# Optimization experiments

Measured on AMD Instinct MI355X. Metric: run time of the kernel, lower is better.

The kernel has to match this reference:

```python
import jax, jax.numpy as jnp
import numpy as np

S = 2048      # total tokens
DIM = 1024    # model dim
H = 16        # attention heads
DH = 64       # head dim
BOT = 256     # bottleneck dim
NIMG = 4      # images (equal size)
L = S // NIMG # tokens per image
K = 256       # sparse_k
IH = 4        # indexer heads
ID = 16       # indexer head dim
MAXREL = 64   # hardcoded in module
NBUCK = 2 * MAXREL + 1
GH = IH * 2   # gate MLP hidden (expansion=2)


def setup_inputs() -> dict:
    key = jax.random.key(0)
    ks = jax.random.split(key, 16)
    r = lambda i, sh, s=0.02: jax.random.normal(ks[i], sh, jnp.float32) * s
    return dict(
        hidden_states=jax.random.normal(ks[0], (S, DIM), jnp.float32),
        patch_coords=jax.random.randint(ks[1], (S, 2), 0, 64, dtype=jnp.int32),
        cu_seqlens=jnp.arange(NIMG + 1, dtype=jnp.int32) * L,
        rotary_pos_emb=jax.random.uniform(ks[2], (S, DH // 2), jnp.float32) * 3.0,
        Wq_idx=r(3, (2 * IH * ID, DIM)),
        Wk_idx=r(4, (2 * IH * ID, DIM)),
        W1g=r(5, (GH, IH)), b1g=jnp.zeros((GH,), jnp.float32),
        W2g=r(6, (IH, GH)), b2g=jnp.zeros((IH,), jnp.float32),
        rpe_table=r(7, (NBUCK, IH)),
        Wqkv_d=r(8, (BOT, DIM)), bqkv_d=jnp.zeros((BOT,), jnp.float32),
        Wqkv_u=r(9, (3 * DIM, BOT)), bqkv_u=jnp.zeros((3 * DIM,), jnp.float32),
        Wp_d=r(10, (BOT, DIM)), bp_d=jnp.zeros((BOT,), jnp.float32),
        Wp_u=r(11, (DIM, BOT)), bp_u=jnp.zeros((DIM,), jnp.float32),
        scaler=jnp.ones((1,), jnp.float32),
    )


def _rotate_half(x):
    x1, x2 = jnp.split(x, 2, axis=-1)
    return jnp.concatenate([-x2, x1], axis=-1)


def reference(hidden_states, patch_coords, cu_seqlens, rotary_pos_emb,
              Wq_idx, Wk_idx, W1g, b1g, W2g, b2g, rpe_table,
              Wqkv_d, bqkv_d, Wqkv_u, bqkv_u, Wp_d, bp_d, Wp_u, bp_u, scaler):
    n = cu_seqlens.shape[0] - 1            # images (equal size L)
    Li = hidden_states.shape[0] // n
    neg = jnp.finfo(hidden_states.dtype).min

    # QKV via low-rank bottleneck
    qkv = (hidden_states @ Wqkv_d.T + bqkv_d) @ Wqkv_u.T + bqkv_u  # [S, 3*DIM]
    qkv = qkv.reshape(S, 3, H, DH)
    q, k, v = qkv[:, 0], qkv[:, 1], qkv[:, 2]                      # [S, H, DH]

    # vision RoPE (emb = cat(rpe, rpe))
    emb = jnp.concatenate([rotary_pos_emb, rotary_pos_emb], axis=-1)  # [S, DH]
    cos = jnp.cos(emb)[:, None, :]
    sin = jnpp if False else jnp.sin(emb)[:, None, :]
    q = q * cos + _rotate_half(q) * sin
    k = k * cos + _rotate_half(k) * sin

    # ---- interaction indexer, vmapped over equal-size images ----
    xs = hidden_states.reshape(n, Li, DIM)
    pos = patch_coords[:, 1].reshape(n, Li).astype(jnp.float32)
    qI = (xs @ Wq_idx.T).reshape(n, Li, 2 * IH, ID)
    kI = (xs @ Wk_idx.T).reshape(n, Li, 2 * IH, ID)
    dot = jnp.einsum('nqhd,nkhd->nqkh', qI, kI)                    # [n, L, L, 2*IH]
    data_in, gate_in = dot[..., :IH], dot[..., IH:]
    rel = jnp.clip(pos[:, :, None] - pos[:, None, :], -MAXREL, MAXREL)
    bucket = (rel + MAXREL).astype(jnp.int32)                      # [n, L, L]
    rpe = rpe_table[bucket]                                        # [n, L, L, IH]
    relu_scores = jax.nn.relu(data_in + rpe)
    g = jax.nn.sigmoid(jax.nn.relu((gate_in + rpe) @ W1g.T + b1g) @ W2g.T + b2g)
    index_scores = (relu_scores * g).sum(-1)                       # [n, L, L]

    # top-k sparse mask (0 at selected keys, -inf-ish elsewhere)
    _, topk_idx = jax.lax.top_k(index_scores, K)                   # [n, L, K]
    ni = jnp.arange(n)[:, None, None]
    ri = jnp.arange(Li)[None, :, None]
    mask_local = jnp.full((n, Li, Li), neg, hidden_states.dtype).at[ni, ri, topk_idx].set(0.0)

    # block-diagonal full mask
    mask = jnp.full((S, S), neg, hidden_states.dtype)
    for i in range(n):
        mask = mask.at[i * Li:(i + 1) * Li, i * Li:(i + 1) * Li].set(mask_local[i])

    # dense SDPA with additive mask
    att = jnp.einsum('qhd,khd->hqk', q, k) / jnp.sqrt(jnp.float32(DH)).astype(q.dtype)
    att = att + mask[None]
    p = jax.nn.softmax(att, axis=-1)
    out = jnp.einsum('hqk,khd->qhd', p, v).reshape(S, H * DH)

    final = (out @ Wp_d.T + bp_d) @ Wp_u.T + bp_u
    return final * scaler
```

## Files before the change

### kernel.cpp

```cpp
#include <hip/hip_runtime.h>
#include <hip/hip_bf16.h>

#define S_    2048
#define DIM_  1024
#define H_    16
#define DH_   64
#define BOT_  256
#define NIMG_ 4
#define LI_   512
#define K_    256
#define IH_   4
#define ID_   16
#define MAXREL_ 64
#define NBUCK_ 129
#define GH_   8
#define IDH2_ 128

typedef short bf16x8 __attribute__((ext_vector_type(8)));
typedef float f32x4  __attribute__((ext_vector_type(4)));

__device__ __forceinline__ unsigned short f2bf(float x) {
    unsigned u = __float_as_uint(x);
    return (unsigned short)((u + 0x7fffu + ((u >> 16) & 1u)) >> 16);
}
__device__ __forceinline__ float bf2f(unsigned short h) {
    return __uint_as_float(((unsigned)h) << 16);
}

#define OFF_W1_    2097152
#define OFF_WQ_    2359296
#define OFF_WK_    2490368
#define OFF_WQKVU_ 2621440
#define OFF_WPD_   3407872
#define OFF_WPU_   3670016
#define NSPLIT_    3932160

__global__ __launch_bounds__(256) void split_all_kernel(
    const float* __restrict__ hid, const float* __restrict__ wqd,
    const float* __restrict__ wq,  const float* __restrict__ wk,
    const float* __restrict__ wqu, const float* __restrict__ wpd,
    const float* __restrict__ wpu,
    unsigned short* __restrict__ hi, unsigned short* __restrict__ lo)
{
    long e = ((long)blockIdx.x * 256 + threadIdx.x) * 4;
    if (e >= NSPLIT_) return;
    const float* src; long off;
    if (e < OFF_W1_)         { src = hid; off = 0; }
    else if (e < OFF_WQ_)    { src = wqd; off = OFF_W1_; }
    else if (e < OFF_WK_)    { src = wq;  off = OFF_WQ_; }
    else if (e < OFF_WQKVU_) { src = wk;  off = OFF_WK_; }
    else if (e < OFF_WPD_)   { src = wqu; off = OFF_WQKVU_; }
    else if (e < OFF_WPU_)   { src = wpd; off = OFF_WPD_; }
    else                     { src = wpu; off = OFF_WPU_; }
    float4 v = *(const float4*)(src + (e - off));
    ushort4 h, l;
    h.x = f2bf(v.x); l.x = f2bf(v.x - bf2f(h.x));
    h.y = f2bf(v.y); l.y = f2bf(v.y - bf2f(h.y));
    h.z = f2bf(v.z); l.z = f2bf(v.z - bf2f(h.z));
    h.w = f2bf(v.w); l.w = f2bf(v.w - bf2f(h.w));
    *(ushort4*)&hi[e] = h;
    *(ushort4*)&lo[e] = l;
}

__global__ __launch_bounds__(256) void gemm_bf16x3(
    const unsigned short* __restrict__ Ah, const unsigned short* __restrict__ Al,
    const unsigned short* __restrict__ Bh, const unsigned short* __restrict__ Bl,
    const float* __restrict__ bias, const float* __restrict__ scale_ptr,
    float* __restrict__ Cf, int M, int N, int Kd)
{
    __shared__ unsigned short sAh[128 * 40], sAl[128 * 40];
    __shared__ unsigned short sBh[64 * 40],  sBl[64 * 40];
    int tid = threadIdx.x;
    int lane = tid & 63, wv = tid >> 6;
    int wr = wv >> 1, wc = wv & 1;
    int row0 = blockIdx.y * 128, col0 = blockIdx.x * 64;

    f32x4 acc[4][2];
#pragma unroll
    for (int i = 0; i < 4; i++)
#pragma unroll
        for (int j = 0; j < 2; j++) acc[i][j] = (f32x4){0.f, 0.f, 0.f, 0.f};

    int ar = tid >> 1, ac = (tid & 1) * 16;
    int br = tid >> 2, bc = (tid & 3) * 8;
    const unsigned short* gAh = Ah + (size_t)(row0 + ar) * Kd + ac;
    const unsigned short* gAl = Al + (size_t)(row0 + ar) * Kd + ac;
    const unsigned short* gBh = Bh + (size_t)(col0 + br) * Kd + bc;
    const unsigned short* gBl = Bl + (size_t)(col0 + br) * Kd + bc;
    int am = lane & 15, qk = (lane >> 4) * 8;

    for (int k0 = 0; k0 < Kd; k0 += 32) {
        __syncthreads();
        *(float4*)&sAh[ar * 40 + ac]     = *(const float4*)(gAh + k0);
        *(float4*)&sAh[ar * 40 + ac + 8] = *(const float4*)(gAh + k0 + 8);
        *(float4*)&sAl[ar * 40 + ac]     = *(const float4*)(gAl + k0);
        *(float4*)&sAl[ar * 40 + ac + 8] = *(const float4*)(gAl + k0 + 8);
        *(float4*)&sBh[br * 40 + bc]     = *(const float4*)(gBh + k0);
        *(float4*)&sBl[br * 40 + bc]     = *(const float4*)(gBl + k0);
        __syncthreads();

        bf16x8 ah[4], al[4], bh[2], bl[2];
#pragma unroll
        for (int rt = 0; rt < 4; rt++) {
            int r = wr * 64 + rt * 16 + am;
            ah[rt] = *(const bf16x8*)&sAh[r * 40 + qk];
            al[rt] = *(const bf16x8*)&sAl[r * 40 + qk];
        }
#pragma unroll
        for (int ct = 0; ct < 2; ct++) {
            int c = wc * 32 + ct * 16 + am;
            bh[ct] = *(const bf16x8*)&sBh[c * 40 + qk];
            bl[ct] = *(const bf16x8*)&sBl[c * 40 + qk];
        }
#pragma unroll
        for (int rt = 0; rt < 4; rt++)
#pragma unroll
            for (int ct = 0; ct < 2; ct++) {
                acc[rt][ct] = __builtin_amdgcn_mfma_f32_16x16x32_bf16(ah[rt], bh[ct], acc[rt][ct], 0, 0, 0);
                acc[rt][ct] = __builtin_amdgcn_mfma_f32_16x16x32_bf16(ah[rt], bl[ct], acc[rt][ct], 0, 0, 0);
                acc[rt][ct] = __builtin_amdgcn_mfma_f32_16x16x32_bf16(al[rt], bh[ct], acc[rt][ct], 0, 0, 0);
            }
    }

    float scl = scale_ptr ? *scale_ptr : 1.0f;
    int rq = (lane >> 4) * 4;
#pragma unroll
    for (int rt = 0; rt < 4; rt++)
#pragma unroll
        for (int ct = 0; ct < 2; ct++) {
            int col = col0 + wc * 32 + ct * 16 + am;
            float bz = bias ? bias[col] : 0.0f;
#pragma unroll
            for (int rg = 0; rg < 4; rg++) {
                int row = row0 + wr * 64 + rt * 16 + rq + rg;
                Cf[(size_t)row * N + col] = (acc[rt][ct][rg] + bz) * scl;
            }
        }
}

__global__ __launch_bounds__(256) void gemm64_bf16x3(
    const unsigned short* __restrict__ Ah, const unsigned short* __restrict__ Al,
    const unsigned short* __restrict__ Bh, const unsigned short* __restrict__ Bl,
    const float* __restrict__ bias_lo, const float* __restrict__ bias_hi,
    float* __restrict__ Cf, unsigned short* __restrict__ Chi,
    unsigned short* __restrict__ Clo, int M, int N, int Kd, int split_col)
{
    __shared__ unsigned short sAh[64 * 72], sAl[64 * 72];
    __shared__ unsigned short sBh[64 * 72], sBl[64 * 72];
    int tid = threadIdx.x;
    int lane = tid & 63, wv = tid >> 6;
    int wr = wv >> 1, wc = wv & 1;
    int row0 = blockIdx.y * 64, col0 = blockIdx.x * 64;

    f32x4 acc[2][2];
#pragma unroll
    for (int i = 0; i < 2; i++)
#pragma unroll
        for (int j = 0; j < 2; j++) acc[i][j] = (f32x4){0.f, 0.f, 0.f, 0.f};

    int sr = tid >> 2, sc = (tid & 3) * 16;
    const unsigned short* gAh = Ah + (size_t)(row0 + sr) * Kd + sc;
    const unsigned short* gAl = Al + (size_t)(row0 + sr) * Kd + sc;
    const unsigned short* gBh = Bh + (size_t)(col0 + sr) * Kd + sc;
    const unsigned short* gBl = Bl + (size_t)(col0 + sr) * Kd + sc;
    int am = lane & 15, qk = (lane >> 4) * 8;

    for (int k0 = 0; k0 < Kd; k0 += 64) {
        __syncthreads();
        *(float4*)&sAh[sr * 72 + sc]     = *(const float4*)(gAh + k0);
        *(float4*)&sAh[sr * 72 + sc + 8] = *(const float4*)(gAh + k0 + 8);
        *(float4*)&sAl[sr * 72 + sc]     = *(const float4*)(gAl + k0);
        *(float4*)&sAl[sr * 72 + sc + 8] = *(const float4*)(gAl + k0 + 8);
        *(float4*)&sBh[sr * 72 + sc]     = *(const float4*)(gBh + k0);
        *(float4*)&sBh[sr * 72 + sc + 8] = *(const float4*)(gBh + k0 + 8);
        *(float4*)&sBl[sr * 72 + sc]     = *(const float4*)(gBl + k0);
        *(float4*)&sBl[sr * 72 + sc + 8] = *(const float4*)(gBl + k0 + 8);
        __syncthreads();

#pragma unroll
        for (int ks = 0; ks < 2; ks++) {
            bf16x8 ah[2], al[2], bh[2], bl[2];
#pragma unroll
            for (int rt = 0; rt < 2; rt++) {
                int r = wr * 32 + rt * 16 + am;
                ah[rt] = *(const bf16x8*)&sAh[r * 72 + ks * 32 + qk];
                al[rt] = *(const bf16x8*)&sAl[r * 72 + ks * 32 + qk];
            }
#pragma unroll
            for (int ct = 0; ct < 2; ct++) {
                int c = wc * 32 + ct * 16 + am;
                bh[ct] = *(const bf16x8*)&sBh[c * 72 + ks * 32 + qk];
                bl[ct] = *(const bf16x8*)&sBl[c * 72 + ks * 32 + qk];
            }
#pragma unroll
            for (int rt = 0; rt < 2; rt++)
#pragma unroll
                for (int ct = 0; ct < 2; ct++) {
                    acc[rt][ct] = __builtin_amdgcn_mfma_f32_16x16x32_bf16(ah[rt], bh[ct], acc[rt][ct], 0, 0, 0);
                    acc[rt][ct] = __builtin_amdgcn_mfma_f32_16x16x32_bf16(ah[rt], bl[ct], acc[rt][ct], 0, 0, 0);
                    acc[rt][ct] = __builtin_amdgcn_mfma_f32_16x16x32_bf16(al[rt], bh[ct], acc[rt][ct], 0, 0, 0);
                }
        }
    }

    int rq = (lane >> 4) * 4;
#pragma unroll
    for (int rt = 0; rt < 2; rt++)
#pragma unroll
        for (int ct = 0; ct < 2; ct++) {
            int col = col0 + wc * 32 + ct * 16 + am;
#pragma unroll
            for (int rg = 0; rg < 4; rg++) {
                int row = row0 + wr * 32 + rt * 16 + rq + rg;
                float v = acc[rt][ct][rg];
                if (col < split_col) {
                    if (bias_lo) v += bias_lo[col];
                    size_t idx = (size_t)row * split_col + col;
                    unsigned short hh = f2bf(v);
                    Chi[idx] = hh;
                    Clo[idx] = f2bf(v - bf2f(hh));
                } else {
                    if (bias_hi) v += bias_hi[col - split_col];
                    Cf[(size_t)row * (N - split_col) + col - split_col] = v;
                }
            }
        }
}

__global__ __launch_bounds__(256) void ropesplit_kernel(
    const float* __restrict__ qkv, const float* __restrict__ rope,
    unsigned short* __restrict__ qkvh, unsigned short* __restrict__ qkvl)
{
    int idx = blockIdx.x * 256 + threadIdx.x;
    int d = idx & 63;
    int hh = (idx >> 6) & (H_ - 1);
    int s = idx >> 10;
    size_t base = (size_t)s * 3072 + hh * 64 + d;
    float q = qkv[base];
    float k = qkv[base + 1024];
    float v = qkv[base + 2048];
    float r = rope[s * 32 + (d & 31)];
    float c = cosf(r), sn = sinf(r);
    float qp = __shfl_xor(q, 32, 64);
    float kp = __shfl_xor(k, 32, 64);
    float sgn = (d < 32) ? -1.0f : 1.0f;
    float qr = (q * c + sgn * qp * sn) * 0.125f;
    float kr = k * c + sgn * kp * sn;
    unsigned short h1 = f2bf(qr);
    qkvh[base] = h1;            qkvl[base] = f2bf(qr - bf2f(h1));
    unsigned short h2 = f2bf(kr);
    qkvh[base + 1024] = h2;     qkvl[base + 1024] = f2bf(kr - bf2f(h2));
    unsigned short h3 = f2bf(v);
    qkvh[base + 2048] = h3;     qkvl[base + 2048] = f2bf(v - bf2f(h3));
}

__global__ __launch_bounds__(256) void score_topk_kernel(
    const float* __restrict__ qIk,
    const int* __restrict__ coords, const float* __restrict__ rpe_table,
    const float* __restrict__ W1g, const float* __restrict__ b1g,
    const float* __restrict__ W2g, const float* __restrict__ b2g,
    unsigned* __restrict__ selmask)
{
    __shared__ unsigned skeys[4][LI_];
    __shared__ int shist[4][256];
    __shared__ float srpe[NBUCK_ * IH_];
    __shared__ float sW1[GH_ * IH_], sb1[GH_], sW2[IH_ * GH_], sb2[IH_];

    int tid  = threadIdx.x;
    int lane = tid & 63;
    int wv   = tid >> 6;
    int row  = blockIdx.x * 4 + wv;
    int n    = row >> 9;

    for (int i = tid; i < NBUCK_ * IH_; i += 256) srpe[i] = rpe_table[i];
    if (tid < 32) sW1[tid] = W1g[tid];
    else if (tid < 64) sW2[tid - 32] = W2g[tid - 32];
    else if (tid < 72) sb1[tid - 64] = b1g[tid - 64];
    else if (tid < 76) sb2[tid - 72] = b2g[tid - 72];

    float4 qv[32];
    {
        const float* qrow = qIk + (size_t)row * 256;
#pragma unroll
        for (int i = 0; i < 32; i++) qv[i] = *(const float4*)(qrow + 4 * i);
    }
    int pq = coords[row * 2 + 1];
    __syncthreads();

    const float* kbase = qIk + (size_t)n * LI_ * 256 + 128;
    for (int kt = 0; kt < 8; kt++) {
        int kg = kt * 64 + lane;
        const float* krow = kbase + (size_t)kg * 256;

        float dh[8];
#pragma unroll
        for (int hh = 0; hh < 8; hh++) {
            float acc = 0.0f;
#pragma unroll
            for (int dq = 0; dq < 4; dq++) {
                float4 kv = *(const float4*)(krow + hh * 16 + dq * 4);
                float4 qq = qv[hh * 4 + dq];
                acc += qq.x * kv.x + qq.y * kv.y + qq.z * kv.z + qq.w * kv.w;
            }
            dh[hh] = acc;
        }
        int pk = coords[(n * LI_ + kg) * 2 + 1];
        int rel = pq - pk;
        rel = rel < -MAXREL_ ? -MAXREL_ : (rel > MAXREL_ ? MAXREL_ : rel);
        const float* rp = srpe + (rel + MAXREL_) * IH_;
        float t1[GH_];
#pragma unroll
        for (int g = 0; g < GH_; g++) t1[g] = sb1[g];
#pragma unroll
        for (int j = 0; j < IH_; j++) {
            float gate = dh[IH_ + j] + rp[j];
#pragma unroll
            for (int g = 0; g < GH_; g++) t1[g] += gate * sW1[g * IH_ + j];
        }
#pragma unroll
        for (int g = 0; g < GH_; g++) t1[g] = fmaxf(t1[g], 0.0f);
        float score = 0.0f;
#pragma unroll
        for (int j = 0; j < IH_; j++) {
            float t2 = sb2[j];
#pragma unroll
            for (int g = 0; g < GH_; g++) t2 += t1[g] * sW2[j * GH_ + g];
            float sg = 1.0f / (1.0f + expf(-t2));
            float rs = fmaxf(dh[j] + rp[j], 0.0f);
            score += rs * sg;
        }
        unsigned bits = __float_as_uint(score);
        skeys[wv][kg] = (bits & 0x80000000u) ? ~bits : (bits | 0x80000000u);
    }
    __syncthreads();

    unsigned pref = 0u;
    int kcur = K_;
    const unsigned himask[4] = {0u, 0xFF000000u, 0xFFFF0000u, 0xFFFFFF00u};
#pragma unroll
    for (int pass = 0; pass < 4; pass++) {
        int shift = 24 - pass * 8;
        unsigned hm = himask[pass];
        *(int4*)&shist[wv][4 * lane] = make_int4(0, 0, 0, 0);
        __syncthreads();
#pragma unroll
        for (int c = 0; c < 8; c++) {
            unsigned key = skeys[wv][c * 64 + lane];
            if ((key & hm) == pref) atomicAdd(&shist[wv][(key >> shift) & 255], 1);
        }
        __syncthreads();
        int4 b4 = *(const int4*)&shist[wv][4 * lane];
        int b[4] = {b4.x, b4.y, b4.z, b4.w};
        int t = b[0] + b[1] + b[2] + b[3];
        int Ssum = t;
#pragma unroll
        for (int off = 1; off < 64; off <<= 1) {
            int u = __shfl_down(Ssum, off, 64);
            if (lane + off < 64) Ssum += u;
        }
        int E = Ssum - t;
        int cs[5];
        cs[4] = E;
        cs[3] = b[3] + E;
        cs[2] = b[2] + cs[3];
        cs[1] = b[1] + cs[2];
        cs[0] = b[0] + cs[1];
        bool found = false;
        unsigned cpref = 0u; int ck = 0;
#pragma unroll
        for (int j = 0; j < 4; j++) {
            if (!found && cs[j] >= kcur && cs[j + 1] < kcur) {
                found = true;
                cpref = pref | ((unsigned)(4 * lane + j) << shift);
                ck = kcur - cs[j + 1];
            }
        }
        unsigned long long bm = __ballot(found);
        int src = __ffsll((long long)bm) - 1;
        pref = (unsigned)__shfl((int)cpref, src, 64);
        kcur = __shfl(ck, src, 64);
        __syncthreads();
    }
    unsigned Tu = pref;

    unsigned long long bg[8], be[8];
#pragma unroll
    for (int c = 0; c < 8; c++) {
        unsigned key = skeys[wv][c * 64 + lane];
        bg[c] = __ballot(key > Tu);
        be[c] = __ballot(key == Tu);
    }
    if (lane < 16) {
        int total_gt = 0;
#pragma unroll
        for (int c = 0; c < 8; c++) total_gt += __popcll(bg[c]);
        int base = 0;
#pragma unroll
        for (int c = 0; c < 8; c++) {
            if (2 * c < lane)     base += __popc((unsigned)be[c]);
            if (2 * c + 1 < lane) base += __popc((unsigned)(be[c] >> 32));
        }
        unsigned gw = (unsigned)(bg[lane >> 1] >> (32 * (lane & 1)));
        unsigned ew = (unsigned)(be[lane >> 1] >> (32 * (lane & 1)));
        int ne = K_ - total_gt - base;
        int pc = __popc(ew);
        int m = ne < 0 ? 0 : (ne > pc ? pc : ne);
        while (pc > m) { ew ^= (1u << (31 - __clz(ew))); pc--; }
        selmask[(size_t)row * 16 + lane] = gw | ew;
    }
}

__global__ __launch_bounds__(256) void attn_kernel(
    const unsigned short* __restrict__ qkvh, const unsigned short* __restrict__ qkvl,
    const unsigned* __restrict__ selmask,
    unsigned short* __restrict__ outh, unsigned short* __restrict__ outl)
{
    __shared__ unsigned short Qh[64 * 72],  Ql[64 * 72];
    __shared__ unsigned short Kh[64 * 72],  Kl[64 * 72];
    __shared__ unsigned short VTh[64 * 72], VTl[64 * 72];
    __shared__ unsigned short Ph[64 * 72],  Pl[64 * 72];
    __shared__ unsigned Ms[64][16];

    int b  = blockIdx.x;
    int qt = b >> 6;
    int nh = b & 63;
    int h  = nh & 15;
    int n  = nh >> 4;
    int tid = threadIdx.x;
    int lane = tid & 63, w = tid >> 6;
    int lane15 = lane & 15, quad = lane >> 4;
    int q0 = n * LI_ + qt * 64;

    for (int i = tid; i < 64 * 16; i += 256)
        Ms[i >> 4][i & 15] = selmask[(size_t)(q0 + (i >> 4)) * 16 + (i & 15)];

    {
        int r = tid >> 2, c0 = (tid & 3) * 16;
        size_t off = (size_t)(q0 + r) * 3072 + h * 64 + c0;
        *(uint4*)&Qh[r * 72 + c0]     = *(const uint4*)(qkvh + off);
        *(uint4*)&Qh[r * 72 + c0 + 8] = *(const uint4*)(qkvh + off + 8);
        *(uint4*)&Ql[r * 72 + c0]     = *(const uint4*)(qkvl + off);
        *(uint4*)&Ql[r * 72 + c0 + 8] = *(const uint4*)(qkvl + off + 8);
    }

    f32x4 o_acc[4];
#pragma unroll
    for (int i = 0; i < 4; i++) o_acc[i] = (f32x4){0.f, 0.f, 0.f, 0.f};
    float rsum[4] = {};

    for (int kt = 0; kt < 8; kt++) {
        __syncthreads();
        {
            int r = tid >> 2, c0 = (tid & 3) * 16;
            size_t off = (size_t)(n * LI_ + kt * 64 + r) * 3072 + 1024 + h * 64 + c0;
            *(uint4*)&Kh[r * 72 + c0]     = *(const uint4*)(qkvh + off);
            *(uint4*)&Kh[r * 72 + c0 + 8] = *(const uint4*)(qkvh + off + 8);
            *(uint4*)&Kl[r * 72 + c0]     = *(const uint4*)(qkvl + off);
            *(uint4*)&Kl[r * 72 + c0 + 8] = *(const uint4*)(qkvl + off + 8);
        }
        {
            int dd = lane;
            int k0 = w * 16;
            size_t off = (size_t)(n * LI_ + kt * 64 + k0) * 3072 + 2048 + h * 64 + dd;
            unsigned short hb[16], lb[16];
#pragma unroll
            for (int j = 0; j < 16; j++) {
                hb[j] = qkvh[off + (size_t)j * 3072];
                lb[j] = qkvl[off + (size_t)j * 3072];
            }
            *(uint4*)&VTh[dd * 72 + k0]     = *(uint4*)&hb[0];
            *(uint4*)&VTh[dd * 72 + k0 + 8] = *(uint4*)&hb[8];
            *(uint4*)&VTl[dd * 72 + k0]     = *(uint4*)&lb[0];
            *(uint4*)&VTl[dd * 72 + k0 + 8] = *(uint4*)&lb[8];
        }
        __syncthreads();

        f32x4 s_acc[4];
#pragma unroll
        for (int nt = 0; nt < 4; nt++) s_acc[nt] = (f32x4){0.f, 0.f, 0.f, 0.f};
        {
            bf16x8 qfh[2], qfl[2];
#pragma unroll
            for (int ks = 0; ks < 2; ks++) {
                qfh[ks] = *(const bf16x8*)&Qh[(16 * w + lane15) * 72 + ks * 32 + quad * 8];
                qfl[ks] = *(const bf16x8*)&Ql[(16 * w + lane15) * 72 + ks * 32 + quad * 8];
            }
#pragma unroll
            for (int nt = 0; nt < 4; nt++) {
#pragma unroll
                for (int ks = 0; ks < 2; ks++) {
                    bf16x8 kfh = *(const bf16x8*)&Kh[(16 * nt + lane15) * 72 + ks * 32 + quad * 8];
                    bf16x8 kfl = *(const bf16x8*)&Kl[(16 * nt + lane15) * 72 + ks * 32 + quad * 8];
                    s_acc[nt] = __builtin_amdgcn_mfma_f32_16x16x32_bf16(qfh[ks], kfh, s_acc[nt], 0, 0, 0);
                    s_acc[nt] = __builtin_amdgcn_mfma_f32_16x16x32_bf16(qfh[ks], kfl, s_acc[nt], 0, 0, 0);
                    s_acc[nt] = __builtin_amdgcn_mfma_f32_16x16x32_bf16(qfl[ks], kfh, s_acc[nt], 0, 0, 0);
                }
            }
        }

#pragma unroll
        for (int nt = 0; nt < 4; nt++) {
            int kb = kt * 64 + nt * 16 + lane15;
            int wi = kb >> 5, bit = kb & 31;
#pragma unroll
            for (int reg = 0; reg < 4; reg++) {
                int qloc = 16 * w + quad * 4 + reg;
                unsigned mw = Ms[qloc][wi];
                float p = ((mw >> bit) & 1u) ? __expf(s_acc[nt][reg]) : 0.0f;
                rsum[reg] += p;
                unsigned short ph = f2bf(p);
                Ph[qloc * 72 + nt * 16 + lane15] = ph;
                Pl[qloc * 72 + nt * 16 + lane15] = f2bf(p - bf2f(ph));
            }
        }

        {
            bf16x8 pfh[2], pfl[2];
#pragma unroll
            for (int ks = 0; ks < 2; ks++) {
                pfh[ks] = *(const bf16x8*)&Ph[(16 * w + lane15) * 72 + ks * 32 + quad * 8];
                pfl[ks] = *(const bf16x8*)&Pl[(16 * w + lane15) * 72 + ks * 32 + quad * 8];
            }
#pragma unroll
            for (int dt = 0; dt < 4; dt++) {
#pragma unroll
                for (int ks = 0; ks < 2; ks++) {
                    bf16x8 vfh = *(const bf16x8*)&VTh[(16 * dt + lane15) * 72 + ks * 32 + quad * 8];
                    bf16x8 vfl = *(const bf16x8*)&VTl[(16 * dt + lane15) * 72 + ks * 32 + quad * 8];
                    o_acc[dt] = __builtin_amdgcn_mfma_f32_16x16x32_bf16(pfh[ks], vfh, o_acc[dt], 0, 0, 0);
                    o_acc[dt] = __builtin_amdgcn_mfma_f32_16x16x32_bf16(pfh[ks], vfl, o_acc[dt], 0, 0, 0);
                    o_acc[dt] = __builtin_amdgcn_mfma_f32_16x16x32_bf16(pfl[ks], vfh, o_acc[dt], 0, 0, 0);
                }
            }
        }
    }

#pragma unroll
    for (int reg = 0; reg < 4; reg++) {
        rsum[reg] += __shfl_xor(rsum[reg], 1, 64);
        rsum[reg] += __shfl_xor(rsum[reg], 2, 64);
        rsum[reg] += __shfl_xor(rsum[reg], 4, 64);
        rsum[reg] += __shfl_xor(rsum[reg], 8, 64);
    }

#pragma unroll
    for (int dt = 0; dt < 4; dt++) {
#pragma unroll
        for (int reg = 0; reg < 4; reg++) {
            float v = o_acc[dt][reg] / rsum[reg];
            size_t ob = (size_t)(q0 + 16 * w + quad * 4 + reg) * 1024 + h * 64 + 16 * dt + lane15;
            unsigned short hh = f2bf(v);
            outh[ob] = hh;
            outl[ob] = f2bf(v - bf2f(hh));
        }
    }
}

extern "C" void kernel_launch(void* const* d_in, const int* in_sizes, int n_in,
                              void* d_out, int out_size, void* d_ws, size_t ws_size,
                              hipStream_t stream)
{
    const float* hidden  = (const float*)d_in[0];
    const int*   coords  = (const int*)d_in[1];
    const float* rope    = (const float*)d_in[3];
    const float* Wq_idx  = (const float*)d_in[4];
    const float* Wk_idx  = (const float*)d_in[5];
    const float* W1g     = (const float*)d_in[6];
    const float* b1g     = (const float*)d_in[7];
    const float* W2g     = (const float*)d_in[8];
    const float* b2g     = (const float*)d_in[9];
    const float* rpe     = (const float*)d_in[10];
    const float* Wqkv_d  = (const float*)d_in[11];
    const float* bqkv_d  = (const float*)d_in[12];
    const float* Wqkv_u  = (const float*)d_in[13];
    const float* bqkv_u  = (const float*)d_in[14];
    const float* Wp_d    = (const float*)d_in[15];
    const float* bp_d    = (const float*)d_in[16];
    const float* Wp_u    = (const float*)d_in[17];
    const float* bp_u    = (const float*)d_in[18];
    const float* scaler  = (const float*)d_in[19];
    float* out = (float*)d_out;

    unsigned short* sp_hi  = (unsigned short*)d_ws;
    unsigned short* sp_lo  = sp_hi + NSPLIT_;
    unsigned short* mid_hi = sp_lo + NSPLIT_;
    unsigned short* mid_lo = mid_hi + (size_t)S_ * BOT_;
    float* qkv = (float*)(mid_lo + (size_t)S_ * BOT_);
    float* qIk = qkv + (size_t)S_ * 3 * DIM_;
    unsigned* selmask = (unsigned*)(qIk + (size_t)S_ * 256);
    unsigned short* qkvh = (unsigned short*)(selmask + (size_t)S_ * 16);
    unsigned short* qkvl = qkvh + (size_t)S_ * 3 * DIM_;

    split_all_kernel<<<(NSPLIT_ / 4 + 255) / 256, 256, 0, stream>>>(
        hidden, Wqkv_d, Wq_idx, Wk_idx, Wqkv_u, Wp_d, Wp_u, sp_hi, sp_lo);

    gemm64_bf16x3<<<dim3(512 / 64, S_ / 64), 256, 0, stream>>>(
        sp_hi, sp_lo, sp_hi + OFF_W1_, sp_lo + OFF_W1_,
        bqkv_d, nullptr, qIk, mid_hi, mid_lo, S_, 512, DIM_, 256);

    score_topk_kernel<<<S_ / 4, 256, 0, stream>>>(
        qIk, coords, rpe, W1g, b1g, W2g, b2g, selmask);

    gemm_bf16x3<<<dim3(3 * DIM_ / 64, S_ / 128), 256, 0, stream>>>(
        mid_hi, mid_lo, sp_hi + OFF_WQKVU_, sp_lo + OFF_WQKVU_,
        bqkv_u, nullptr, qkv, S_, 3 * DIM_, BOT_);

    ropesplit_kernel<<<(S_ * H_ * 64) / 256, 256, 0, stream>>>(
        qkv, rope, qkvh, qkvl);

    attn_kernel<<<NIMG_ * H_ * 8, 256, 0, stream>>>(qkvh, qkvl, selmask, sp_hi, sp_lo);

    gemm64_bf16x3<<<dim3(BOT_ / 64, S_ / 64), 256, 0, stream>>>(
        sp_hi, sp_lo, sp_hi + OFF_WPD_, sp_lo + OFF_WPD_,
        bp_d, nullptr, nullptr, mid_hi, mid_lo, S_, BOT_, DIM_, BOT_);

    gemm_bf16x3<<<dim3(DIM_ / 64, S_ / 128), 256, 0, stream>>>(
        mid_hi, mid_lo, sp_hi + OFF_WPU_, sp_lo + OFF_WPU_,
        bp_u, scaler, out, S_, DIM_, BOT_);
}
```

Before: 290.4 us.

## Write transposed indexer keys from GEMM epilogue and drop wave-local syncs in top-k

The first bottleneck GEMM now writes the indexer-key half of its output transposed, one [n, dim, key] plane per image, into a new workspace buffer. The score kernel then reads keys so that adjacent lanes touch adjacent addresses, replacing per-lane strided float4 row reads. Query vectors move from a 32-float4 register array into shared memory, which lowers register pressure. Block-wide barriers around the per-wave histogram radix select are removed because each wave uses only its own shared slices. Risks are that the new buffer extends past the old workspace end and that correctness now relies on wave-level ordering of the shared-memory histogram accesses.

```diff
diff --git a/kernel.cpp b/kernel.cpp
--- a/kernel.cpp
+++ b/kernel.cpp
@@ -142,7 +142,8 @@
     const unsigned short* __restrict__ Ah, const unsigned short* __restrict__ Al,
     const unsigned short* __restrict__ Bh, const unsigned short* __restrict__ Bl,
     const float* __restrict__ bias_lo, const float* __restrict__ bias_hi,
-    float* __restrict__ Cf, unsigned short* __restrict__ Chi,
+    float* __restrict__ Cf, float* __restrict__ CfT,
+    unsigned short* __restrict__ Chi,
     unsigned short* __restrict__ Clo, int M, int N, int Kd, int split_col)
 {
     __shared__ unsigned short sAh[64 * 72], sAl[64 * 72];
@@ -209,17 +210,30 @@
 #pragma unroll
         for (int ct = 0; ct < 2; ct++) {
             int col = col0 + wc * 32 + ct * 16 + am;
-#pragma unroll
-            for (int rg = 0; rg < 4; rg++) {
-                int row = row0 + wr * 32 + rt * 16 + rq + rg;
-                float v = acc[rt][ct][rg];
-                if (col < split_col) {
+            if (col < split_col) {
+#pragma unroll
+                for (int rg = 0; rg < 4; rg++) {
+                    int row = row0 + wr * 32 + rt * 16 + rq + rg;
+                    float v = acc[rt][ct][rg];
                     if (bias_lo) v += bias_lo[col];
                     size_t idx = (size_t)row * split_col + col;
                     unsigned short hh = f2bf(v);
                     Chi[idx] = hh;
                     Clo[idx] = f2bf(v - bf2f(hh));
-                } else {
+                }
+            } else if (CfT && col >= split_col + 128) {
+                int d = col - split_col - 128;
+                int rowb = row0 + wr * 32 + rt * 16 + rq;
+                int n = row0 >> 9;
+                int key0 = rowb & (LI_ - 1);
+                float4 vv = make_float4(acc[rt][ct][0], acc[rt][ct][1],
+                                        acc[rt][ct][2], acc[rt][ct][3]);
+                *(float4*)&CfT[(size_t)(n * 128 + d) * LI_ + key0] = vv;
+            } else {
+#pragma unroll
+                for (int rg = 0; rg < 4; rg++) {
+                    int row = row0 + wr * 32 + rt * 16 + rq + rg;
+                    float v = acc[rt][ct][rg];
                     if (bias_hi) v += bias_hi[col - split_col];
                     Cf[(size_t)row * (N - split_col) + col - split_col] = v;
                 }
@@ -255,12 +269,13 @@
 }
 
 __global__ __launch_bounds__(256) void score_topk_kernel(
-    const float* __restrict__ qIk,
+    const float* __restrict__ qIk, const float* __restrict__ kIT,
     const int* __restrict__ coords, const float* __restrict__ rpe_table,
     const float* __restrict__ W1g, const float* __restrict__ b1g,
     const float* __restrict__ W2g, const float* __restrict__ b2g,
     unsigned* __restrict__ selmask)
 {
+    __shared__ float sqI2[4][IDH2_];
     __shared__ unsigned skeys[4][LI_];
     __shared__ int shist[4][256];
     __shared__ float srpe[NBUCK_ * IH_];
@@ -277,20 +292,18 @@
     else if (tid < 64) sW2[tid - 32] = W2g[tid - 32];
     else if (tid < 72) sb1[tid - 64] = b1g[tid - 64];
     else if (tid < 76) sb2[tid - 72] = b2g[tid - 72];
-
-    float4 qv[32];
-    {
-        const float* qrow = qIk + (size_t)row * 256;
-#pragma unroll
-        for (int i = 0; i < 32; i++) qv[i] = *(const float4*)(qrow + 4 * i);
-    }
+    for (int i = tid; i < 4 * IDH2_; i += 256)
+        sqI2[i >> 7][i & 127] =
+            qIk[(size_t)(blockIdx.x * 4 + (i >> 7)) * 256 + (i & 127)];
     int pq = coords[row * 2 + 1];
     __syncthreads();
 
-    const float* kbase = qIk + (size_t)n * LI_ * 256 + 128;
+    const float* kb = kIT + (size_t)n * 128 * LI_;
+    const float* sq = &sqI2[wv][0];
+
     for (int kt = 0; kt < 8; kt++) {
         int kg = kt * 64 + lane;
-        const float* krow = kbase + (size_t)kg * 256;
+        const float* kp = kb + kg;
 
         float dh[8];
 #pragma unroll
@@ -298,9 +311,13 @@
             float acc = 0.0f;
 #pragma unroll
             for (int dq = 0; dq < 4; dq++) {
-                float4 kv = *(const float4*)(krow + hh * 16 + dq * 4);
-                float4 qq = qv[hh * 4 + dq];
-                acc += qq.x * kv.x + qq.y * kv.y + qq.z * kv.z + qq.w * kv.w;
+                int d = hh * 16 + dq * 4;
+                float k0 = kp[(size_t)(d + 0) * LI_];
+                float k1 = kp[(size_t)(d + 1) * LI_];
+                float k2 = kp[(size_t)(d + 2) * LI_];
+                float k3 = kp[(size_t)(d + 3) * LI_];
+                acc += sq[d + 0] * k0 + sq[d + 1] * k1 +
+                       sq[d + 2] * k2 + sq[d + 3] * k3;
             }
             dh[hh] = acc;
         }
@@ -332,7 +349,6 @@
         unsigned bits = __float_as_uint(score);
         skeys[wv][kg] = (bits & 0x80000000u) ? ~bits : (bits | 0x80000000u);
     }
-    __syncthreads();
 
     unsigned pref = 0u;
     int kcur = K_;
@@ -342,13 +358,11 @@
         int shift = 24 - pass * 8;
         unsigned hm = himask[pass];
         *(int4*)&shist[wv][4 * lane] = make_int4(0, 0, 0, 0);
-        __syncthreads();
 #pragma unroll
         for (int c = 0; c < 8; c++) {
             unsigned key = skeys[wv][c * 64 + lane];
             if ((key & hm) == pref) atomicAdd(&shist[wv][(key >> shift) & 255], 1);
         }
-        __syncthreads();
         int4 b4 = *(const int4*)&shist[wv][4 * lane];
         int b[4] = {b4.x, b4.y, b4.z, b4.w};
         int t = b[0] + b[1] + b[2] + b[3];
@@ -379,7 +393,6 @@
         int src = __ffsll((long long)bm) - 1;
         pref = (unsigned)__shfl((int)cpref, src, 64);
         kcur = __shfl(ck, src, 64);
-        __syncthreads();
     }
     unsigned Tu = pref;
 
@@ -590,16 +603,17 @@
     unsigned* selmask = (unsigned*)(qIk + (size_t)S_ * 256);
     unsigned short* qkvh = (unsigned short*)(selmask + (size_t)S_ * 16);
     unsigned short* qkvl = qkvh + (size_t)S_ * 3 * DIM_;
+    float* kIT = (float*)(qkvl + (size_t)S_ * 3 * DIM_);
 
     split_all_kernel<<<(NSPLIT_ / 4 + 255) / 256, 256, 0, stream>>>(
         hidden, Wqkv_d, Wq_idx, Wk_idx, Wqkv_u, Wp_d, Wp_u, sp_hi, sp_lo);
 
     gemm64_bf16x3<<<dim3(512 / 64, S_ / 64), 256, 0, stream>>>(
         sp_hi, sp_lo, sp_hi + OFF_W1_, sp_lo + OFF_W1_,
-        bqkv_d, nullptr, qIk, mid_hi, mid_lo, S_, 512, DIM_, 256);
+        bqkv_d, nullptr, qIk, kIT, mid_hi, mid_lo, S_, 512, DIM_, 256);
 
     score_topk_kernel<<<S_ / 4, 256, 0, stream>>>(
-        qIk, coords, rpe, W1g, b1g, W2g, b2g, selmask);
+        qIk, kIT, coords, rpe, W1g, b1g, W2g, b2g, selmask);
 
     gemm_bf16x3<<<dim3(3 * DIM_ / 64, S_ / 128), 256, 0, stream>>>(
         mid_hi, mid_lo, sp_hi + OFF_WQKVU_, sp_lo + OFF_WQKVU_,
@@ -612,7 +626,7 @@
 
     gemm64_bf16x3<<<dim3(BOT_ / 64, S_ / 64), 256, 0, stream>>>(
         sp_hi, sp_lo, sp_hi + OFF_WPD_, sp_lo + OFF_WPD_,
-        bp_d, nullptr, nullptr, mid_hi, mid_lo, S_, BOT_, DIM_, BOT_);
+        bp_d, nullptr, nullptr, nullptr, mid_hi, mid_lo, S_, BOT_, DIM_, BOT_);
 
     gemm_bf16x3<<<dim3(DIM_ / 64, S_ / 128), 256, 0, stream>>>(
         mid_hi, mid_lo, sp_hi + OFF_WPU_, sp_lo + OFF_WPU_,
```

After: 356.2 us. 22.7% more time.

## Stage indexer key tiles in shared memory with double buffering in score_topk

Applied to the files above, without the earlier changes.

The score_topk kernel now loads 32-key tiles of indexer keys into double-buffered shared memory, shared by all four waves of a block, instead of each wave streaming its keys from global memory. Each half-wave computes four of the eight head dot products, and the halves swap results with cross-lane shuffles. The query row is staged in LDS rather than kept in 128 registers, which frees registers. The per-wave radix-select histogram passes drop their block-wide barriers, and the kernel launch moves after the rope kernel. The trade-off is two barriers per tile and a gate MLP that both half-waves compute redundantly.

```diff
diff --git a/kernel.cpp b/kernel.cpp
--- a/kernel.cpp
+++ b/kernel.cpp
@@ -261,6 +261,8 @@
     const float* __restrict__ W2g, const float* __restrict__ b2g,
     unsigned* __restrict__ selmask)
 {
+    __shared__ float skI[2][32 * 132];
+    __shared__ float sqI2[4][IDH2_];
     __shared__ unsigned skeys[4][LI_];
     __shared__ int shist[4][256];
     __shared__ float srpe[NBUCK_ * IH_];
@@ -277,33 +279,64 @@
     else if (tid < 64) sW2[tid - 32] = W2g[tid - 32];
     else if (tid < 72) sb1[tid - 64] = b1g[tid - 64];
     else if (tid < 76) sb2[tid - 72] = b2g[tid - 72];
-
-    float4 qv[32];
+    for (int i = tid; i < 4 * IDH2_; i += 256)
+        sqI2[i >> 7][i & 127] =
+            qIk[(size_t)(blockIdx.x * 4 + (i >> 7)) * 256 + (i & 127)];
+    int pq = coords[row * 2 + 1];
+
+    const float* kbg = qIk + (size_t)n * LI_ * 256 + 128;
+
     {
-        const float* qrow = qIk + (size_t)row * 256;
-#pragma unroll
-        for (int i = 0; i < 32; i++) qv[i] = *(const float4*)(qrow + 4 * i);
-    }
-    int pq = coords[row * 2 + 1];
+#pragma unroll
+        for (int j = 0; j < 4; j++) {
+            int f = j * 256 + tid;
+            int key = f >> 5, c = f & 31;
+            float4 v = *(const float4*)(kbg + (size_t)key * 256 + 4 * c);
+            *(float4*)&skI[0][key * 132 + 4 * c] = v;
+        }
+    }
     __syncthreads();
 
-    const float* kbase = qIk + (size_t)n * LI_ * 256 + 128;
-    for (int kt = 0; kt < 8; kt++) {
-        int kg = kt * 64 + lane;
-        const float* krow = kbase + (size_t)kg * 256;
-
+    int half = lane >> 5, k5 = lane & 31;
+    const float* sq = &sqI2[wv][0];
+
+    for (int t = 0; t < 16; t++) {
+        int cur = t & 1;
+        float4 pre[4];
+        if (t < 15) {
+#pragma unroll
+            for (int j = 0; j < 4; j++) {
+                int f = j * 256 + tid;
+                int key = f >> 5, c = f & 31;
+                pre[j] = *(const float4*)(kbg + (size_t)((t + 1) * 32 + key) * 256 + 4 * c);
+            }
+        }
+
+        float dh4[4];
+        const float* kp = &skI[cur][k5 * 132];
+#pragma unroll
+        for (int hh = 0; hh < 4; hh++) {
+            int h = 4 * half + hh;
+            float acc = 0.0f;
+#pragma unroll
+            for (int dq = 0; dq < 4; dq++) {
+                float4 kv = *(const float4*)(kp + h * 16 + dq * 4);
+                const float* sqp = sq + h * 16 + dq * 4;
+                acc += sqp[0] * kv.x + sqp[1] * kv.y + sqp[2] * kv.z + sqp[3] * kv.w;
+            }
+            dh4[hh] = acc;
+        }
+        float oth[4];
+#pragma unroll
+        for (int j = 0; j < 4; j++) oth[j] = __shfl_xor(dh4[j], 32, 64);
         float dh[8];
 #pragma unroll
-        for (int hh = 0; hh < 8; hh++) {
-            float acc = 0.0f;
-#pragma unroll
-            for (int dq = 0; dq < 4; dq++) {
-                float4 kv = *(const float4*)(krow + hh * 16 + dq * 4);
-                float4 qq = qv[hh * 4 + dq];
-                acc += qq.x * kv.x + qq.y * kv.y + qq.z * kv.z + qq.w * kv.w;
-            }
-            dh[hh] = acc;
-        }
+        for (int j = 0; j < 4; j++) {
+            dh[j]     = half ? oth[j] : dh4[j];
+            dh[4 + j] = half ? dh4[j] : oth[j];
+        }
+
+        int kg = t * 32 + k5;
         int pk = coords[(n * LI_ + kg) * 2 + 1];
         int rel = pq - pk;
         rel = rel < -MAXREL_ ? -MAXREL_ : (rel > MAXREL_ ? MAXREL_ : rel);
@@ -330,9 +363,20 @@
             score += rs * sg;
         }
         unsigned bits = __float_as_uint(score);
-        skeys[wv][kg] = (bits & 0x80000000u) ? ~bits : (bits | 0x80000000u);
-    }
-    __syncthreads();
+        unsigned keyv = (bits & 0x80000000u) ? ~bits : (bits | 0x80000000u);
+        if (half == 0) skeys[wv][kg] = keyv;
+
+        __syncthreads();
+        if (t < 15) {
+#pragma unroll
+            for (int j = 0; j < 4; j++) {
+                int f = j * 256 + tid;
+                int key = f >> 5, c = f & 31;
+                *(float4*)&skI[cur ^ 1][key * 132 + 4 * c] = pre[j];
+            }
+        }
+        __syncthreads();
+    }
 
     unsigned pref = 0u;
     int kcur = K_;
@@ -342,13 +386,11 @@
         int shift = 24 - pass * 8;
         unsigned hm = himask[pass];
         *(int4*)&shist[wv][4 * lane] = make_int4(0, 0, 0, 0);
-        __syncthreads();
 #pragma unroll
         for (int c = 0; c < 8; c++) {
             unsigned key = skeys[wv][c * 64 + lane];
             if ((key & hm) == pref) atomicAdd(&shist[wv][(key >> shift) & 255], 1);
         }
-        __syncthreads();
         int4 b4 = *(const int4*)&shist[wv][4 * lane];
         int b[4] = {b4.x, b4.y, b4.z, b4.w};
         int t = b[0] + b[1] + b[2] + b[3];
@@ -379,7 +421,6 @@
         int src = __ffsll((long long)bm) - 1;
         pref = (unsigned)__shfl((int)cpref, src, 64);
         kcur = __shfl(ck, src, 64);
-        __syncthreads();
     }
     unsigned Tu = pref;
 
@@ -598,9 +639,6 @@
         sp_hi, sp_lo, sp_hi + OFF_W1_, sp_lo + OFF_W1_,
         bqkv_d, nullptr, qIk, mid_hi, mid_lo, S_, 512, DIM_, 256);
 
-    score_topk_kernel<<<S_ / 4, 256, 0, stream>>>(
-        qIk, coords, rpe, W1g, b1g, W2g, b2g, selmask);
-
     gemm_bf16x3<<<dim3(3 * DIM_ / 64, S_ / 128), 256, 0, stream>>>(
         mid_hi, mid_lo, sp_hi + OFF_WQKVU_, sp_lo + OFF_WQKVU_,
         bqkv_u, nullptr, qkv, S_, 3 * DIM_, BOT_);
@@ -608,6 +646,9 @@
     ropesplit_kernel<<<(S_ * H_ * 64) / 256, 256, 0, stream>>>(
         qkv, rope, qkvh, qkvl);
 
+    score_topk_kernel<<<S_ / 4, 256, 0, stream>>>(
+        qIk, coords, rpe, W1g, b1g, W2g, b2g, selmask);
+
     attn_kernel<<<NIMG_ * H_ * 8, 256, 0, stream>>>(qkvh, qkvl, selmask, sp_hi, sp_lo);
 
     gemm64_bf16x3<<<dim3(BOT_ / 64, S_ / 64), 256, 0, stream>>>(
```

After: 261.7 us. 9.9% less time.
